# Kernel tuning notes

Measured on AMD Instinct MI355X. Metric: run time of the kernel, lower is better.

Reference implementation:

```python
import jax, jax.numpy as jnp
import numpy as np

D_MODEL, D_K, H = 1024, 64, 16
B, S = 2, 2048

def setup_inputs() -> dict:
    key = jax.random.key(0)
    ks = jax.random.split(key, 9)
    s_in = 1.0 / np.sqrt(D_MODEL)
    x = jax.random.normal(ks[0], (B, S, D_MODEL), dtype=jnp.float32)
    Wq = jax.random.uniform(ks[1], (H, D_MODEL, D_K), jnp.float32, -s_in, s_in)
    bq = jax.random.uniform(ks[2], (H, D_K), jnp.float32, -s_in, s_in)
    Wk = jax.random.uniform(ks[3], (H, D_MODEL, D_K), jnp.float32, -s_in, s_in)
    bk = jax.random.uniform(ks[4], (H, D_K), jnp.float32, -s_in, s_in)
    Wv = jax.random.uniform(ks[5], (H, D_MODEL, D_K), jnp.float32, -s_in, s_in)
    bv = jax.random.uniform(ks[6], (H, D_K), jnp.float32, -s_in, s_in)
    Wo = jax.random.uniform(ks[7], (D_MODEL, D_MODEL), jnp.float32, -s_in, s_in)
    bo = jax.random.uniform(ks[8], (D_MODEL,), jnp.float32, -s_in, s_in)
    return {"x": x, "Wq": Wq, "bq": bq, "Wk": Wk, "bk": bk,
            "Wv": Wv, "bv": bv, "Wo": Wo, "bo": bo}

def reference(x, Wq, bq, Wk, bk, Wv, bv, Wo, bo):
    # PositionLinear = Linear + ReLU (the ReLU is part of the original math)
    Q = jax.nn.relu(jnp.einsum('bsd,hdk->bhsk', x, Wq) + bq[:, None, :])
    K = jax.nn.relu(jnp.einsum('bsd,hdk->bhsk', x, Wk) + bk[:, None, :])
    V = jax.nn.relu(jnp.einsum('bsd,hdk->bhsk', x, Wv) + bv[:, None, :])
    scale = jnp.sqrt(jnp.float32(Q.shape[-1]))
    scores = jnp.einsum('bhsk,bhtk->bhst', Q, K) / scale  # [B,H,S,S]
    attn = jax.nn.softmax(scores, axis=-1)
    ctx = jnp.einsum('bhst,bhtk->bhsk', attn, V)
    # concat heads along feature dim (head order matches torch.cat(output, 2))
    ctx = jnp.transpose(ctx, (0, 2, 1, 3)).reshape(x.shape[0], x.shape[1], -1)
    out = jax.nn.relu(ctx @ Wo + bo)
    return out
```

## Files before the change

kernel.cpp:

```cpp
#include <hip/hip_runtime.h>
#include <cstddef>

#define D_MODEL 1024
#define DK 64
#define NH 16
#define NB 2
#define SEQ 2048

typedef __attribute__((ext_vector_type(8))) short bf16x8;
typedef __attribute__((ext_vector_type(4))) float floatx4;

static __device__ __forceinline__ unsigned short f2bf(float f) {
    union { float f; unsigned u; } v; v.f = f;
    unsigned r = (v.u + 0x7fffu + ((v.u >> 16) & 1u)) >> 16;
    return (unsigned short)r;
}

static __device__ __forceinline__ unsigned pk2bf(float lo, float hi) {
    unsigned ua = __float_as_uint(lo) + 0x8000u;
    unsigned ub = __float_as_uint(hi) + 0x8000u;
    return __builtin_amdgcn_perm(ub, ua, 0x07060302u);
}

static __device__ __forceinline__ float swz16(float x) {
    return __int_as_float(__builtin_amdgcn_ds_swizzle(__float_as_int(x), 0x401F));
}

static __device__ __forceinline__ void gld16(const unsigned short* g, unsigned short* l) {
    __builtin_amdgcn_global_load_lds(
        (const __attribute__((address_space(1))) unsigned int*)g,
        (__attribute__((address_space(3))) unsigned int*)l, 16, 0, 0);
}

__global__ __launch_bounds__(256) void convert_x(const float* __restrict__ x,
                                                 unsigned short* __restrict__ xb)
{
    const size_t i = ((size_t)blockIdx.x * 256 + threadIdx.x) * 16;
#pragma unroll
    for (int c = 0; c < 16; c += 4) {
        float4 v = *(const float4*)&x[i + c];
        uint2 pk;
        pk.x = (unsigned)f2bf(v.x) | ((unsigned)f2bf(v.y) << 16);
        pk.y = (unsigned)f2bf(v.z) | ((unsigned)f2bf(v.w) << 16);
        *(uint2*)&xb[i + c] = pk;
    }
}

__global__ __launch_bounds__(256) void pack_w(
    const float* __restrict__ Wq, const float* __restrict__ Wk,
    const float* __restrict__ Wv, const float* __restrict__ Wo,
    unsigned short* __restrict__ Bqkv, unsigned short* __restrict__ Bo)
{
    __shared__ float T[64][65];
    const int t   = blockIdx.x;
    const int tid = threadIdx.x;
    const int rr   = tid >> 2;
    const int cseg = (tid & 3) * 16;

    const float* src;
    unsigned short* dst;
    if (t < 768) {
        const int proj = t / 256, rem = t % 256;
        const int h = rem >> 4, d0 = (rem & 15) * 64;
        const float* W = proj == 0 ? Wq : (proj == 1 ? Wk : Wv);
        src = W + ((size_t)h * 1024 + d0) * 64;
#pragma unroll
        for (int c = 0; c < 16; c += 4) {
            float4 v = *(const float4*)&src[(size_t)rr * 64 + cseg + c];
            T[rr][cseg + c + 0] = v.x; T[rr][cseg + c + 1] = v.y;
            T[rr][cseg + c + 2] = v.z; T[rr][cseg + c + 3] = v.w;
        }
        __syncthreads();
        dst = &Bqkv[((size_t)proj * 1024 + h * 64 + rr) * 1024 + d0 + cseg];
    } else {
        const int t2 = t - 768;
        const int k0 = (t2 >> 4) * 64, nb0 = (t2 & 15) * 64;
#pragma unroll
        for (int c = 0; c < 16; c += 4) {
            float4 v = *(const float4*)&Wo[(size_t)(k0 + rr) * 1024 + nb0 + cseg + c];
            T[rr][cseg + c + 0] = v.x; T[rr][cseg + c + 1] = v.y;
            T[rr][cseg + c + 2] = v.z; T[rr][cseg + c + 3] = v.w;
        }
        __syncthreads();
        dst = &Bo[(size_t)(nb0 + rr) * 1024 + k0 + cseg];
    }
    unsigned int w[8];
#pragma unroll
    for (int ii = 0; ii < 8; ii++) {
        unsigned short lo = f2bf(T[cseg + ii * 2 + 0][rr]);
        unsigned short hi = f2bf(T[cseg + ii * 2 + 1][rr]);
        w[ii] = (unsigned)lo | ((unsigned)hi << 16);
    }
    *(uint4*)(dst + 0) = make_uint4(w[0], w[1], w[2], w[3]);
    *(uint4*)(dst + 8) = make_uint4(w[4], w[5], w[6], w[7]);
}

__global__ __launch_bounds__(256) void gemm_qkv(
    const unsigned short* __restrict__ Abf,
    const unsigned short* __restrict__ Bp,
    const float* __restrict__ bq, const float* __restrict__ bk,
    const float* __restrict__ bv,
    unsigned short* __restrict__ Qo, unsigned short* __restrict__ Ko,
    unsigned short* __restrict__ Vo)
{
    __shared__ __align__(16) unsigned short As[128 * 32];
    __shared__ __align__(16) unsigned short Bs[128 * 32];

    const int tid  = threadIdx.x;
    const int wv   = tid >> 6, lane = tid & 63;
    const int m0   = blockIdx.x * 128;
    const int n0   = blockIdx.y * 128;
    const int lq   = lane & 15, g = lane >> 4;
    const int wm   = (wv >> 1) * 64;
    const int wn   = (wv & 1) * 64;
    const int srow = lane >> 2;
    const int sseg = (lane & 3) * 8;

    floatx4 acc[4][4];
#pragma unroll
    for (int i = 0; i < 4; i++)
#pragma unroll
        for (int j = 0; j < 4; j++) acc[i][j] = (floatx4){0.f, 0.f, 0.f, 0.f};

    for (int k0 = 0; k0 < 1024; k0 += 32) {
#pragma unroll
        for (int r = 0; r < 2; r++) {
            const int chunk = wv * 2 + r;
            const int row   = chunk * 16 + srow;
            gld16(&Abf[(size_t)(m0 + row) * 1024 + k0 + sseg], &As[chunk * 512]);
            gld16(&Bp [(size_t)(n0 + row) * 1024 + k0 + sseg], &Bs[chunk * 512]);
        }
        __syncthreads();
        bf16x8 af[4], bfv[4];
#pragma unroll
        for (int i = 0; i < 4; i++)
            af[i] = *(const bf16x8*)&As[(wm + i * 16 + lq) * 32 + g * 8];
#pragma unroll
        for (int j = 0; j < 4; j++)
            bfv[j] = *(const bf16x8*)&Bs[(wn + j * 16 + lq) * 32 + g * 8];
#pragma unroll
        for (int i = 0; i < 4; i++)
#pragma unroll
            for (int j = 0; j < 4; j++)
                acc[i][j] = __builtin_amdgcn_mfma_f32_16x16x32_bf16(af[i], bfv[j], acc[i][j], 0, 0, 0);
        __syncthreads();
    }

    const int proj = n0 >> 10;
    const float* bias = proj == 0 ? bq : (proj == 1 ? bk : bv);
    unsigned short* OutQK = proj == 0 ? Qo : Ko;

#pragma unroll
    for (int j = 0; j < 4; j++) {
        const int n  = n0 + wn + j * 16 + lq;
        const int nn = n & 1023;
        const int h  = nn >> 6, dk = nn & 63;
        const float bb = bias[nn];
#pragma unroll
        for (int i = 0; i < 4; i++) {
            const int mbase = m0 + wm + i * 16 + g * 4;
            const int b_ = mbase >> 11;
            const int s_ = mbase & (SEQ - 1);
            const int bh = b_ * NH + h;
            if (proj < 2) {
                const size_t fb = (((size_t)bh * 128 + (s_ >> 4)) * 2 + (dk >> 5)) * 512
                                + (size_t)((((dk & 31) >> 3) * 16) + (s_ & 15)) * 8 + (dk & 7);
#pragma unroll
                for (int r = 0; r < 4; r++)
                    OutQK[fb + (size_t)r * 8] = f2bf(fmaxf(acc[i][j][r] + bb, 0.f));
            } else {
                const size_t fb = ((((size_t)bh * 32 + (s_ >> 6)) * 4 + (dk >> 4)) * 2
                                   + ((s_ >> 5) & 1)) * 512
                                + (size_t)((((s_ & 31) >> 3) * 16) + (dk & 15)) * 8 + (s_ & 7);
                uint2 pk;
                pk.x = (unsigned)f2bf(fmaxf(acc[i][j][0] + bb, 0.f))
                     | ((unsigned)f2bf(fmaxf(acc[i][j][1] + bb, 0.f)) << 16);
                pk.y = (unsigned)f2bf(fmaxf(acc[i][j][2] + bb, 0.f))
                     | ((unsigned)f2bf(fmaxf(acc[i][j][3] + bb, 0.f)) << 16);
                *(uint2*)&Vo[fb] = pk;
            }
        }
    }
}

__global__ __launch_bounds__(256, 2) void attn_kernel(
    const unsigned short* __restrict__ Qf,
    const unsigned short* __restrict__ Kf,
    const unsigned short* __restrict__ Vf,
    unsigned short* __restrict__ ctxb)
{
    __shared__ __align__(16) unsigned short Ps[4][2][16][72];

    const int blk = blockIdx.x;
    const int xcd = blk & 7;
    const int j_  = blk >> 3;
    const int bh  = xcd * 4 + (j_ & 3);
    const int qt  = j_ >> 2;

    const int tid  = threadIdx.x;
    const int wv   = tid >> 6;
    const int lane = tid & 63;
    const int lq   = lane & 15;
    const int g    = lane >> 4;

    const int q0 = qt * 128 + wv * 32;

    const size_t qfB = ((size_t)bh * 128 + (q0 >> 4)) * 1024 + (size_t)lane * 8;
    bf16x8 q0a = *(const bf16x8*)&Qf[qfB];
    bf16x8 q0b = *(const bf16x8*)&Qf[qfB + 512];
    bf16x8 q1a = *(const bf16x8*)&Qf[qfB + 1024];
    bf16x8 q1b = *(const bf16x8*)&Qf[qfB + 1536];

    const float C  = 0.18033688011112042f;
    const float MC = 2.8853900817779267f;

    float l0 = 0.f, l1 = 0.f;
    floatx4 acc0[4], acc1[4];
#pragma unroll
    for (int i = 0; i < 4; i++) {
        acc0[i] = (floatx4){0.f, 0.f, 0.f, 0.f};
        acc1[i] = (floatx4){0.f, 0.f, 0.f, 0.f};
    }

    for (int jt = 0; jt < SEQ / 64; jt++) {
        const unsigned short* kp = &Kf[((size_t)bh * 128 + jt * 4) * 1024 + (size_t)lane * 8];
        const unsigned short* vp = &Vf[((size_t)bh * 32 + jt) * 4096 + (size_t)lane * 8];

        floatx4 s0[4], s1[4];
#pragma unroll
        for (int mt = 0; mt < 4; mt++) {
            bf16x8 a0 = *(const bf16x8*)(kp + mt * 1024);
            bf16x8 a1 = *(const bf16x8*)(kp + mt * 1024 + 512);
            s0[mt] = (floatx4){0.f, 0.f, 0.f, 0.f};
            s0[mt] = __builtin_amdgcn_mfma_f32_16x16x32_bf16(a0, q0a, s0[mt], 0, 0, 0);
            s0[mt] = __builtin_amdgcn_mfma_f32_16x16x32_bf16(a1, q0b, s0[mt], 0, 0, 0);
            s1[mt] = (floatx4){0.f, 0.f, 0.f, 0.f};
            s1[mt] = __builtin_amdgcn_mfma_f32_16x16x32_bf16(a0, q1a, s1[mt], 0, 0, 0);
            s1[mt] = __builtin_amdgcn_mfma_f32_16x16x32_bf16(a1, q1b, s1[mt], 0, 0, 0);
        }

        bf16x8 vr[8];
#pragma unroll
        for (int nt = 0; nt < 4; nt++) {
            vr[nt]     = *(const bf16x8*)(vp + nt * 1024);
            vr[4 + nt] = *(const bf16x8*)(vp + nt * 1024 + 512);
        }

#pragma unroll
        for (int mt = 0; mt < 4; mt++) {
            float p00 = __builtin_amdgcn_exp2f(fmaf(s0[mt][0], C, -MC));
            float p01 = __builtin_amdgcn_exp2f(fmaf(s0[mt][1], C, -MC));
            float p02 = __builtin_amdgcn_exp2f(fmaf(s0[mt][2], C, -MC));
            float p03 = __builtin_amdgcn_exp2f(fmaf(s0[mt][3], C, -MC));
            l0 += (p00 + p01) + (p02 + p03);
            uint2 pk;
            pk.x = pk2bf(p00, p01);
            pk.y = pk2bf(p02, p03);
            *(uint2*)&Ps[wv][0][lq][mt * 16 + g * 4] = pk;
            float p10 = __builtin_amdgcn_exp2f(fmaf(s1[mt][0], C, -MC));
            float p11 = __builtin_amdgcn_exp2f(fmaf(s1[mt][1], C, -MC));
            float p12 = __builtin_amdgcn_exp2f(fmaf(s1[mt][2], C, -MC));
            float p13 = __builtin_amdgcn_exp2f(fmaf(s1[mt][3], C, -MC));
            l1 += (p10 + p11) + (p12 + p13);
            uint2 pk1;
            pk1.x = pk2bf(p10, p11);
            pk1.y = pk2bf(p12, p13);
            *(uint2*)&Ps[wv][1][lq][mt * 16 + g * 4] = pk1;
        }
        __builtin_amdgcn_s_waitcnt(0xC07F);
        bf16x8 pb00 = *(const bf16x8*)&Ps[wv][0][lq][g * 8];
        bf16x8 pb01 = *(const bf16x8*)&Ps[wv][0][lq][32 + g * 8];
        bf16x8 pb10 = *(const bf16x8*)&Ps[wv][1][lq][g * 8];
        bf16x8 pb11 = *(const bf16x8*)&Ps[wv][1][lq][32 + g * 8];

#pragma unroll
        for (int nt = 0; nt < 4; nt++) {
            acc0[nt] = __builtin_amdgcn_mfma_f32_16x16x32_bf16(vr[nt],     pb00, acc0[nt], 0, 0, 0);
            acc0[nt] = __builtin_amdgcn_mfma_f32_16x16x32_bf16(vr[4 + nt], pb01, acc0[nt], 0, 0, 0);
            acc1[nt] = __builtin_amdgcn_mfma_f32_16x16x32_bf16(vr[nt],     pb10, acc1[nt], 0, 0, 0);
            acc1[nt] = __builtin_amdgcn_mfma_f32_16x16x32_bf16(vr[4 + nt], pb11, acc1[nt], 0, 0, 0);
        }
    }

    l0 += swz16(l0); l0 += __shfl_xor(l0, 32, 64);
    l1 += swz16(l1); l1 += __shfl_xor(l1, 32, 64);
    const float li0 = 1.f / l0, li1 = 1.f / l1;
    const int b_ = bh >> 4, h_ = bh & 15;
#pragma unroll
    for (int nt = 0; nt < 4; nt++) {
        uint2 pk;
        pk.x = pk2bf(acc0[nt][0] * li0, acc0[nt][1] * li0);
        pk.y = pk2bf(acc0[nt][2] * li0, acc0[nt][3] * li0);
        *(uint2*)&ctxb[((size_t)(b_ * SEQ) + q0 + lq) * D_MODEL + h_ * DK + nt * 16 + g * 4] = pk;
        uint2 pk1;
        pk1.x = pk2bf(acc1[nt][0] * li1, acc1[nt][1] * li1);
        pk1.y = pk2bf(acc1[nt][2] * li1, acc1[nt][3] * li1);
        *(uint2*)&ctxb[((size_t)(b_ * SEQ) + q0 + 16 + lq) * D_MODEL + h_ * DK + nt * 16 + g * 4] = pk1;
    }
}

__global__ __launch_bounds__(256) void gemm_o(
    const unsigned short* __restrict__ Abf,
    const unsigned short* __restrict__ Bp,
    const float* __restrict__ bo,
    float* __restrict__ out)
{
    __shared__ __align__(16) unsigned short As[128 * 32];
    __shared__ __align__(16) unsigned short Bs[128 * 32];

    const int tid  = threadIdx.x;
    const int wv   = tid >> 6, lane = tid & 63;
    const int m0   = blockIdx.x * 128;
    const int n0   = blockIdx.y * 128;
    const int lq   = lane & 15, g = lane >> 4;
    const int wm   = (wv >> 1) * 64;
    const int wn   = (wv & 1) * 64;
    const int srow = lane >> 2;
    const int sseg = (lane & 3) * 8;

    floatx4 acc[4][4];
#pragma unroll
    for (int i = 0; i < 4; i++)
#pragma unroll
        for (int j = 0; j < 4; j++) acc[i][j] = (floatx4){0.f, 0.f, 0.f, 0.f};

    for (int k0 = 0; k0 < 1024; k0 += 32) {
#pragma unroll
        for (int r = 0; r < 2; r++) {
            const int chunk = wv * 2 + r;
            const int row   = chunk * 16 + srow;
            gld16(&Abf[(size_t)(m0 + row) * 1024 + k0 + sseg], &As[chunk * 512]);
            gld16(&Bp [(size_t)(n0 + row) * 1024 + k0 + sseg], &Bs[chunk * 512]);
        }
        __syncthreads();
        bf16x8 af[4], bfv[4];
#pragma unroll
        for (int i = 0; i < 4; i++)
            af[i] = *(const bf16x8*)&As[(wm + i * 16 + lq) * 32 + g * 8];
#pragma unroll
        for (int j = 0; j < 4; j++)
            bfv[j] = *(const bf16x8*)&Bs[(wn + j * 16 + lq) * 32 + g * 8];
#pragma unroll
        for (int i = 0; i < 4; i++)
#pragma unroll
            for (int j = 0; j < 4; j++)
                acc[i][j] = __builtin_amdgcn_mfma_f32_16x16x32_bf16(af[i], bfv[j], acc[i][j], 0, 0, 0);
        __syncthreads();
    }

#pragma unroll
    for (int j = 0; j < 4; j++) {
        const int n  = n0 + wn + j * 16 + lq;
        const float bb = bo[n];
#pragma unroll
        for (int i = 0; i < 4; i++) {
#pragma unroll
            for (int r = 0; r < 4; r++) {
                const int m = m0 + wm + i * 16 + g * 4 + r;
                out[(size_t)m * 1024 + n] = fmaxf(acc[i][j][r] + bb, 0.f);
            }
        }
    }
}

extern "C" void kernel_launch(void* const* d_in, const int* in_sizes, int n_in,
                              void* d_out, int out_size, void* d_ws, size_t ws_size,
                              hipStream_t stream) {
    const float* x  = (const float*)d_in[0];
    const float* Wq = (const float*)d_in[1];
    const float* bq = (const float*)d_in[2];
    const float* Wk = (const float*)d_in[3];
    const float* bk = (const float*)d_in[4];
    const float* Wv = (const float*)d_in[5];
    const float* bv = (const float*)d_in[6];
    const float* Wo = (const float*)d_in[7];
    const float* bo = (const float*)d_in[8];
    float* out = (float*)d_out;

    const size_t perE = (size_t)NB * NH * SEQ * DK;
    unsigned short* xbf  = (unsigned short*)d_ws;
    unsigned short* Bqkv = xbf  + (size_t)4096 * 1024;
    unsigned short* Bo   = Bqkv + (size_t)3072 * 1024;
    unsigned short* Qfr  = Bo   + (size_t)1024 * 1024;
    unsigned short* Kfr  = Qfr + perE;
    unsigned short* Vfr  = Kfr + perE;
    unsigned short* Cbf  = Vfr + perE;

    convert_x<<<1024, 256, 0, stream>>>(x, xbf);
    pack_w<<<1024, 256, 0, stream>>>(Wq, Wk, Wv, Wo, Bqkv, Bo);
    gemm_qkv<<<dim3(32, 24), 256, 0, stream>>>(xbf, Bqkv, bq, bk, bv, Qfr, Kfr, Vfr);
    attn_kernel<<<512, 256, 0, stream>>>(Qfr, Kfr, Vfr, Cbf);
    gemm_o<<<dim3(32, 8), 256, 0, stream>>>(Cbf, Bo, bo, out);
}
```

Measured before the change: 196.7 us.

## Double-buffer K/V tiles in LDS with async global-to-LDS prefetch

The attention loop now stages each 64-key K and V tile into a double-buffered shared-memory region with direct global-to-LDS loads. The next tile is prefetched while the current one is computed. Before, each of the four waves loaded the whole K/V tile from global memory on its own. This shares one load across the block and hides latency, at the cost of 32 KB more LDS (which may reduce occupancy), a block barrier on every iteration, and one redundant wraparound prefetch.

```diff
diff --git a/kernel.cpp b/kernel.cpp
--- a/kernel.cpp
+++ b/kernel.cpp
@@ -189,6 +189,7 @@
     const unsigned short* __restrict__ Vf,
     unsigned short* __restrict__ ctxb)
 {
+    __shared__ __align__(16) unsigned short KVs[2][8192];
     __shared__ __align__(16) unsigned short Ps[4][2][16][72];
 
     const int blk = blockIdx.x;
@@ -214,6 +215,9 @@
     const float C  = 0.18033688011112042f;
     const float MC = 2.8853900817779267f;
 
+    const unsigned short* KtB = &Kf[(size_t)bh * 131072];
+    const unsigned short* VtB = &Vf[(size_t)bh * 131072];
+
     float l0 = 0.f, l1 = 0.f;
     floatx4 acc0[4], acc1[4];
 #pragma unroll
@@ -222,15 +226,35 @@
         acc1[i] = (floatx4){0.f, 0.f, 0.f, 0.f};
     }
 
+#pragma unroll
+    for (int r = 0; r < 2; r++) {
+        const int c = wv * 2 + r;
+        gld16(&KtB[(size_t)c * 512 + lane * 8], &KVs[0][c * 512]);
+        gld16(&VtB[(size_t)c * 512 + lane * 8], &KVs[0][4096 + c * 512]);
+    }
+    __syncthreads();
+
     for (int jt = 0; jt < SEQ / 64; jt++) {
-        const unsigned short* kp = &Kf[((size_t)bh * 128 + jt * 4) * 1024 + (size_t)lane * 8];
-        const unsigned short* vp = &Vf[((size_t)bh * 32 + jt) * 4096 + (size_t)lane * 8];
+        const int buf = jt & 1;
+
+        const int jn = (jt + 1) & (SEQ / 64 - 1);
+        const unsigned short* ktn = &KtB[(size_t)jn * 4096];
+        const unsigned short* vtn = &VtB[(size_t)jn * 4096];
+#pragma unroll
+        for (int r = 0; r < 2; r++) {
+            const int c = wv * 2 + r;
+            gld16(&ktn[(size_t)c * 512 + lane * 8], &KVs[buf ^ 1][c * 512]);
+            gld16(&vtn[(size_t)c * 512 + lane * 8], &KVs[buf ^ 1][4096 + c * 512]);
+        }
+
+        const unsigned short* kb = &KVs[buf][0];
+        const unsigned short* vb = &KVs[buf][4096];
 
         floatx4 s0[4], s1[4];
 #pragma unroll
         for (int mt = 0; mt < 4; mt++) {
-            bf16x8 a0 = *(const bf16x8*)(kp + mt * 1024);
-            bf16x8 a1 = *(const bf16x8*)(kp + mt * 1024 + 512);
+            bf16x8 a0 = *(const bf16x8*)&kb[mt * 1024 + lane * 8];
+            bf16x8 a1 = *(const bf16x8*)&kb[mt * 1024 + 512 + lane * 8];
             s0[mt] = (floatx4){0.f, 0.f, 0.f, 0.f};
             s0[mt] = __builtin_amdgcn_mfma_f32_16x16x32_bf16(a0, q0a, s0[mt], 0, 0, 0);
             s0[mt] = __builtin_amdgcn_mfma_f32_16x16x32_bf16(a1, q0b, s0[mt], 0, 0, 0);
@@ -242,8 +266,8 @@
         bf16x8 vr[8];
 #pragma unroll
         for (int nt = 0; nt < 4; nt++) {
-            vr[nt]     = *(const bf16x8*)(vp + nt * 1024);
-            vr[4 + nt] = *(const bf16x8*)(vp + nt * 1024 + 512);
+            vr[nt]     = *(const bf16x8*)&vb[nt * 1024 + lane * 8];
+            vr[4 + nt] = *(const bf16x8*)&vb[nt * 1024 + 512 + lane * 8];
         }
 
 #pragma unroll
@@ -280,6 +304,8 @@
             acc1[nt] = __builtin_amdgcn_mfma_f32_16x16x32_bf16(vr[nt],     pb10, acc1[nt], 0, 0, 0);
             acc1[nt] = __builtin_amdgcn_mfma_f32_16x16x32_bf16(vr[4 + nt], pb11, acc1[nt], 0, 0, 0);
         }
+
+        __syncthreads();
     }
 
     l0 += swz16(l0); l0 += __shfl_xor(l0, 32, 64);
```

After: 194.9 us. Within noise of the previous version (-0.9%).

## Split attention key range across wave pairs and merge partials in LDS

Applied to the files above, without the earlier changes.

Each attention block now handles 64 queries, with pairs of waves splitting the key sequence in half. The second half's partial accumulators and row sums are added into the first through shared memory before normalisation. The grid doubles to 1024 blocks and the launch bound allows 4 blocks per CU, which increases parallelism on the GPU. In exchange it adds extra LDS usage, a block barrier, and idle waves during the final write.

```diff
diff --git a/kernel.cpp b/kernel.cpp
--- a/kernel.cpp
+++ b/kernel.cpp
@@ -183,13 +183,15 @@
     }
 }
 
-__global__ __launch_bounds__(256, 2) void attn_kernel(
+__global__ __launch_bounds__(256, 4) void attn_kernel(
     const unsigned short* __restrict__ Qf,
     const unsigned short* __restrict__ Kf,
     const unsigned short* __restrict__ Vf,
     unsigned short* __restrict__ ctxb)
 {
     __shared__ __align__(16) unsigned short Ps[4][2][16][72];
+    __shared__ __align__(16) float Cmb[2][8][256];
+    __shared__ float Lmb[2][2][64];
 
     const int blk = blockIdx.x;
     const int xcd = blk & 7;
@@ -202,8 +204,10 @@
     const int lane = tid & 63;
     const int lq   = lane & 15;
     const int g    = lane >> 4;
-
-    const int q0 = qt * 128 + wv * 32;
+    const int qgrp  = wv >> 1;
+    const int khalf = wv & 1;
+
+    const int q0 = qt * 64 + qgrp * 32;
 
     const size_t qfB = ((size_t)bh * 128 + (q0 >> 4)) * 1024 + (size_t)lane * 8;
     bf16x8 q0a = *(const bf16x8*)&Qf[qfB];
@@ -222,9 +226,10 @@
         acc1[i] = (floatx4){0.f, 0.f, 0.f, 0.f};
     }
 
-    for (int jt = 0; jt < SEQ / 64; jt++) {
-        const unsigned short* kp = &Kf[((size_t)bh * 128 + jt * 4) * 1024 + (size_t)lane * 8];
-        const unsigned short* vp = &Vf[((size_t)bh * 32 + jt) * 4096 + (size_t)lane * 8];
+    for (int jt = 0; jt < 16; jt++) {
+        const int kt = khalf * 16 + jt;
+        const unsigned short* kp = &Kf[((size_t)bh * 128 + kt * 4) * 1024 + (size_t)lane * 8];
+        const unsigned short* vp = &Vf[((size_t)bh * 32 + kt) * 4096 + (size_t)lane * 8];
 
         floatx4 s0[4], s1[4];
 #pragma unroll
@@ -282,20 +287,39 @@
         }
     }
 
-    l0 += swz16(l0); l0 += __shfl_xor(l0, 32, 64);
-    l1 += swz16(l1); l1 += __shfl_xor(l1, 32, 64);
-    const float li0 = 1.f / l0, li1 = 1.f / l1;
-    const int b_ = bh >> 4, h_ = bh & 15;
-#pragma unroll
-    for (int nt = 0; nt < 4; nt++) {
-        uint2 pk;
-        pk.x = pk2bf(acc0[nt][0] * li0, acc0[nt][1] * li0);
-        pk.y = pk2bf(acc0[nt][2] * li0, acc0[nt][3] * li0);
-        *(uint2*)&ctxb[((size_t)(b_ * SEQ) + q0 + lq) * D_MODEL + h_ * DK + nt * 16 + g * 4] = pk;
-        uint2 pk1;
-        pk1.x = pk2bf(acc1[nt][0] * li1, acc1[nt][1] * li1);
-        pk1.y = pk2bf(acc1[nt][2] * li1, acc1[nt][3] * li1);
-        *(uint2*)&ctxb[((size_t)(b_ * SEQ) + q0 + 16 + lq) * D_MODEL + h_ * DK + nt * 16 + g * 4] = pk1;
+    if (khalf == 1) {
+#pragma unroll
+        for (int nt = 0; nt < 4; nt++) {
+            *(floatx4*)&Cmb[qgrp][nt][lane * 4]     = acc0[nt];
+            *(floatx4*)&Cmb[qgrp][4 + nt][lane * 4] = acc1[nt];
+        }
+        Lmb[qgrp][0][lane] = l0;
+        Lmb[qgrp][1][lane] = l1;
+    }
+    __syncthreads();
+    if (khalf == 0) {
+#pragma unroll
+        for (int nt = 0; nt < 4; nt++) {
+            acc0[nt] += *(const floatx4*)&Cmb[qgrp][nt][lane * 4];
+            acc1[nt] += *(const floatx4*)&Cmb[qgrp][4 + nt][lane * 4];
+        }
+        l0 += Lmb[qgrp][0][lane];
+        l1 += Lmb[qgrp][1][lane];
+        l0 += swz16(l0); l0 += __shfl_xor(l0, 32, 64);
+        l1 += swz16(l1); l1 += __shfl_xor(l1, 32, 64);
+        const float li0 = 1.f / l0, li1 = 1.f / l1;
+        const int b_ = bh >> 4, h_ = bh & 15;
+#pragma unroll
+        for (int nt = 0; nt < 4; nt++) {
+            uint2 pk;
+            pk.x = pk2bf(acc0[nt][0] * li0, acc0[nt][1] * li0);
+            pk.y = pk2bf(acc0[nt][2] * li0, acc0[nt][3] * li0);
+            *(uint2*)&ctxb[((size_t)(b_ * SEQ) + q0 + lq) * D_MODEL + h_ * DK + nt * 16 + g * 4] = pk;
+            uint2 pk1;
+            pk1.x = pk2bf(acc1[nt][0] * li1, acc1[nt][1] * li1);
+            pk1.y = pk2bf(acc1[nt][2] * li1, acc1[nt][3] * li1);
+            *(uint2*)&ctxb[((size_t)(b_ * SEQ) + q0 + 16 + lq) * D_MODEL + h_ * DK + nt * 16 + g * 4] = pk1;
+        }
     }
 }
 
@@ -389,6 +413,6 @@
     convert_x<<<1024, 256, 0, stream>>>(x, xbf);
     pack_w<<<1024, 256, 0, stream>>>(Wq, Wk, Wv, Wo, Bqkv, Bo);
     gemm_qkv<<<dim3(32, 24), 256, 0, stream>>>(xbf, Bqkv, bq, bk, bv, Qfr, Kfr, Vfr);
-    attn_kernel<<<512, 256, 0, stream>>>(Qfr, Kfr, Vfr, Cbf);
+    attn_kernel<<<1024, 256, 0, stream>>>(Qfr, Kfr, Vfr, Cbf);
     gemm_o<<<dim3(32, 8), 256, 0, stream>>>(Cbf, Bo, bo, out);
 }
```

After: 202.0 us. 1.03x slower.
